# Kernel optimization log

Hardware: AMD Instinct MI355X
Metric: run time of the kernel (lower is better)

Reference implementation:

```python
import jax, jax.numpy as jnp
import numpy as np

B, N, D = 16, 1024, 512
H, KD = 8, 64
SCALE = 1.0 / np.sqrt(KD)


def setup_inputs() -> dict:
    key = jax.random.key(0)
    ks = jax.random.split(key, 6)
    return {
        "x": jax.random.normal(ks[0], (B, N, D), dtype=jnp.float32),
        "leadlag_bias": jax.random.normal(ks[1], (N, N), dtype=jnp.float32),
        "Wq": jax.random.normal(ks[2], (D, H * KD), dtype=jnp.float32) * 0.02,
        "Wk": jax.random.normal(ks[3], (D, H * KD), dtype=jnp.float32) * 0.02,
        "Wv": jax.random.normal(ks[4], (D, H * KD), dtype=jnp.float32) * 0.02,
        "Wo": jax.random.normal(ks[5], (H * KD, D), dtype=jnp.float32) * 0.02,
        "bias_scale": jnp.ones((H,), dtype=jnp.float32),
    }


def reference(x, leadlag_bias, Wq, Wk, Wv, Wo, bias_scale):
    # x: [B, N, D]; project and split heads -> [B, H, N, KD]
    def split_heads(t):
        return t.reshape(B, N, H, KD).transpose(0, 2, 1, 3)

    Q = split_heads(x @ Wq)
    K = split_heads(x @ Wk)
    V = split_heads(x @ Wv)

    # scores: [B, H, N, N] with per-head scaled additive lead-lag bias
    scores = jnp.einsum("bhqd,bhkd->bhqk", Q, K) * SCALE
    scores = scores + leadlag_bias[None, None, :, :] * bias_scale.reshape(1, H, 1, 1)

    attn = jax.nn.softmax(scores, axis=-1)  # dropout rate 0.0 / inference
    out = jnp.einsum("bhqk,bhkd->bhqd", attn, V)
    out = out.transpose(0, 2, 1, 3).reshape(B, N, H * KD)
    return out @ Wo
```

## Files before the change

### kernel.cpp

```cpp
#include <hip/hip_runtime.h>


#define DEV static __device__ __forceinline__

typedef __attribute__((ext_vector_type(8))) __bf16 bf16x8;
typedef __attribute__((ext_vector_type(4))) float f32x4;
typedef __attribute__((ext_vector_type(8))) unsigned short u16x8;

static constexpr float SCALE = 0.125f;
static constexpr float LOG2E = 1.4426950408889634f;
static constexpr float SM_SHIFT = 24.0f;
static constexpr int LDT = 72;

DEV unsigned short f2bf(float f) {
    unsigned int u = __builtin_bit_cast(unsigned int, f);
    u += 0x7FFFu + ((u >> 16) & 1u);
    return (unsigned short)(u >> 16);
}
DEV float bf2f(unsigned short u) {
    return __builtin_bit_cast(float, (unsigned int)u << 16);
}

DEV f32x4 mfma16(bf16x8 a, bf16x8 b, f32x4 c) {
    return __builtin_amdgcn_mfma_f32_16x16x32_bf16(a, b, c, 0, 0, 0);
}

__global__ __launch_bounds__(256) void prep_wt(
    const float* __restrict__ Wq, const float* __restrict__ Wk,
    const float* __restrict__ Wv, const float* __restrict__ Wo,
    const float* __restrict__ bias,
    unsigned short* __restrict__ Wt, unsigned short* __restrict__ Wot,
    unsigned short* __restrict__ BiasB)
{
    const int bid = blockIdx.x;
    const int tid = threadIdx.x;

    if (bid >= 256) {
        const int base = (bid - 256) * 2048 + tid * 8;
        float4 a = *(const float4*)(bias + base);
        float4 b = *(const float4*)(bias + base + 4);
        ushort4 u0 = make_ushort4(f2bf(a.x), f2bf(a.y), f2bf(a.z), f2bf(a.w));
        ushort4 u1 = make_ushort4(f2bf(b.x), f2bf(b.y), f2bf(b.z), f2bf(b.w));
        *(ushort4*)&BiasB[base] = u0;
        *(ushort4*)&BiasB[base + 4] = u1;
        return;
    }

    const int mat  = bid >> 6;
    const int tile = bid & 63;
    const int k0 = (tile >> 3) << 6;
    const int n0 = (tile & 7) << 6;
    const float* src = mat == 0 ? Wq : mat == 1 ? Wk : mat == 2 ? Wv : Wo;
    const float mul = (mat == 0) ? SCALE * LOG2E : 1.0f;

    __shared__ unsigned short T[64 * 68];

    #pragma unroll
    for (int i = 0; i < 4; ++i) {
        int idx = tid + (i << 8);
        int r = idx >> 4, c4 = (idx & 15) << 2;
        float4 v = *(const float4*)(src + (size_t)(k0 + r) * 512 + n0 + c4);
        T[r * 68 + c4 + 0] = f2bf(v.x * mul);
        T[r * 68 + c4 + 1] = f2bf(v.y * mul);
        T[r * 68 + c4 + 2] = f2bf(v.z * mul);
        T[r * 68 + c4 + 3] = f2bf(v.w * mul);
    }
    __syncthreads();
    unsigned short* dst = (mat < 3) ? (Wt + (size_t)(mat * 512) * 512) : Wot;
    #pragma unroll
    for (int i = 0; i < 4; ++i) {
        int idx = tid + (i << 8);
        int nr = idx >> 4, kc4 = (idx & 15) << 2;
        ushort4 u;
        u.x = T[(kc4 + 0) * 68 + nr];
        u.y = T[(kc4 + 1) * 68 + nr];
        u.z = T[(kc4 + 2) * 68 + nr];
        u.w = T[(kc4 + 3) * 68 + nr];
        *(ushort4*)&dst[(size_t)(n0 + nr) * 512 + k0 + kc4] = u;
    }
}

__global__ __launch_bounds__(256) void proj_gemm(
    const float* __restrict__ X,
    const unsigned short* __restrict__ Wt,
    unsigned short* __restrict__ Qb,
    unsigned short* __restrict__ Kb,
    unsigned short* __restrict__ Vtb)
{
    __shared__ unsigned short smem[2 * 128 * LDT];
    unsigned short* As = smem;
    unsigned short* Bs = smem + 128 * LDT;

    const int tid  = threadIdx.x;
    const int lane = tid & 63;
    const int wave = tid >> 6;
    const int wm = wave >> 1, wn = wave & 1;
    const int bm = blockIdx.x & 127, bn = blockIdx.x >> 7;
    const int m0 = bm << 7, n0 = bn << 7;
    const int gcol = lane & 15;
    const int grow = (lane >> 4) << 2;
    const int g8   = (lane >> 4) << 3;

    f32x4 acc[4][4];
    const f32x4 zf = {0.f, 0.f, 0.f, 0.f};
    #pragma unroll
    for (int i = 0; i < 4; ++i)
        #pragma unroll
        for (int j = 0; j < 4; ++j) acc[i][j] = zf;

    for (int kt = 0; kt < 8; ++kt) {
        const int k0 = kt << 6;
        #pragma unroll
        for (int i = 0; i < 8; ++i) {
            int idx = tid + (i << 8);
            int r = idx >> 4, c4 = (idx & 15) << 2;
            float4 v = *(const float4*)(X + (size_t)(m0 + r) * 512 + k0 + c4);
            ushort4 u = make_ushort4(f2bf(v.x), f2bf(v.y), f2bf(v.z), f2bf(v.w));
            *(ushort4*)&As[r * LDT + c4] = u;
            *(ushort4*)&Bs[r * LDT + c4] =
                *(const ushort4*)(Wt + (size_t)(n0 + r) * 512 + k0 + c4);
        }
        __syncthreads();
        #pragma unroll
        for (int ks = 0; ks < 2; ++ks) {
            bf16x8 af[4], bfr[4];
            #pragma unroll
            for (int f = 0; f < 4; ++f) {
                af[f]  = *(const bf16x8*)&As[(wm * 64 + f * 16 + gcol) * LDT + ks * 32 + g8];
                bfr[f] = *(const bf16x8*)&Bs[(wn * 64 + f * 16 + gcol) * LDT + ks * 32 + g8];
            }
            #pragma unroll
            for (int mf = 0; mf < 4; ++mf)
                #pragma unroll
                for (int nf = 0; nf < 4; ++nf)
                    acc[mf][nf] = mfma16(af[mf], bfr[nf], acc[mf][nf]);
        }
        __syncthreads();
    }

    const int sect = n0 >> 9;
    const int nq   = n0 & 511;
    const int b    = m0 >> 10;
    const int qb   = m0 & 1023;

    if (sect < 2) {
        unsigned short* dst = (sect == 0) ? Qb : Kb;
        #pragma unroll
        for (int mf = 0; mf < 4; ++mf)
            #pragma unroll
            for (int nf = 0; nf < 4; ++nf) {
                int ncol = nq + wn * 64 + nf * 16;
                int h = ncol >> 6;
                int d = (ncol & 63) + gcol;
                int q = qb + wm * 64 + mf * 16 + grow;
                unsigned short* p = dst + ((size_t)((b * 8 + h) * 1024 + q)) * 64 + d;
                #pragma unroll
                for (int r = 0; r < 4; ++r) p[r * 64] = f2bf(acc[mf][nf][r]);
            }
    } else {
        unsigned short* Ct = smem;
        const int CTP = 130;
        #pragma unroll
        for (int mf = 0; mf < 4; ++mf)
            #pragma unroll
            for (int nf = 0; nf < 4; ++nf) {
                int rr = wm * 64 + mf * 16 + grow;
                int cc = wn * 64 + nf * 16 + gcol;
                #pragma unroll
                for (int r = 0; r < 4; ++r)
                    Ct[(rr + r) * CTP + cc] = f2bf(acc[mf][nf][r]);
            }
        __syncthreads();
        const int qloc = tid & 127, half = tid >> 7;
        for (int it = 0; it < 64; ++it) {
            int dl = it * 2 + half;
            int ncol = nq + dl;
            int h = ncol >> 6, d = ncol & 63;
            Vtb[((size_t)((b * 8 + h) * 64 + d)) * 1024 + qb + qloc] = Ct[qloc * CTP + dl];
        }
    }
}

__global__ __launch_bounds__(256, 4) void attn_kernel(
    const unsigned short* __restrict__ Qb,
    const unsigned short* __restrict__ Kb,
    const unsigned short* __restrict__ Vtb,
    const unsigned short* __restrict__ BiasB,
    const float* __restrict__ bscale,
    unsigned short* __restrict__ AO)
{
    __shared__ unsigned short Klds[64 * LDT];
    __shared__ unsigned short Vlds[64 * LDT];
    __shared__ unsigned short Plds[128 * LDT];

    const int bid = blockIdx.x;
    const int G  = bid & 127;
    const int qt = bid >> 7;
    const int h  = G & 7, b = G >> 3;
    const int q0 = qt << 7;
    const int tid  = threadIdx.x;
    const int lane = tid & 63;
    const int wave = tid >> 6;
    const int wq   = wave << 5;
    const int gcol = lane & 15;
    const int grow = (lane >> 4) << 2;
    const int g8   = (lane >> 4) << 3;

    const float bs = bscale[h] * LOG2E;
    const unsigned short* Qp = Qb + ((size_t)((b * 8 + h) * 1024 + q0)) * 64;
    const unsigned short* Kp = Kb + (size_t)(b * 8 + h) * 1024 * 64;
    const unsigned short* Vp = Vtb + (size_t)(b * 8 + h) * 64 * 1024;
    const unsigned short* Bp = BiasB + (size_t)(q0 + wq) * 1024;

    #pragma unroll
    for (int i = 0; i < 4; ++i) {
        int idx = tid + (i << 8);
        int r = idx >> 3, c8 = (idx & 7) << 3;
        *(u16x8*)&Plds[r * LDT + c8] = *(const u16x8*)&Qp[(size_t)r * 64 + c8];
    }
    __syncthreads();
    bf16x8 qf[2][2];
    #pragma unroll
    for (int mf = 0; mf < 2; ++mf)
        #pragma unroll
        for (int ks = 0; ks < 2; ++ks)
            qf[mf][ks] = *(const bf16x8*)&Plds[(wq + mf * 16 + gcol) * LDT + ks * 32 + g8];
    __syncthreads();

    const f32x4 zf = {0.f, 0.f, 0.f, 0.f};
    f32x4 O[2][4];
    float psum[2][4];
    #pragma unroll
    for (int mf = 0; mf < 2; ++mf) {
        #pragma unroll
        for (int df = 0; df < 4; ++df) O[mf][df] = zf;
        #pragma unroll
        for (int r = 0; r < 4; ++r) psum[mf][r] = 0.f;
    }

    for (int t = 0; t < 16; ++t) {
        const int k0 = t << 6;
        #pragma unroll
        for (int i = 0; i < 2; ++i) {
            int idx = tid + (i << 8);
            int r = idx >> 3, c8 = (idx & 7) << 3;
            *(u16x8*)&Klds[r * LDT + c8] = *(const u16x8*)&Kp[(size_t)(k0 + r) * 64 + c8];
            *(u16x8*)&Vlds[r * LDT + c8] = *(const u16x8*)&Vp[(size_t)r * 1024 + k0 + c8];
        }
        #pragma unroll
        for (int pass = 0; pass < 4; ++pass) {
            int rl = (lane >> 3) + (pass << 3);
            int c8 = (lane & 7) << 3;
            *(u16x8*)&Plds[(wq + rl) * LDT + c8] =
                *(const u16x8*)&Bp[(size_t)rl * 1024 + k0 + c8];
        }
        __syncthreads();

        f32x4 s[2][4];
        #pragma unroll
        for (int mf = 0; mf < 2; ++mf)
            #pragma unroll
            for (int f = 0; f < 4; ++f) s[mf][f] = zf;
        #pragma unroll
        for (int ks = 0; ks < 2; ++ks) {
            bf16x8 kf_[4];
            #pragma unroll
            for (int f = 0; f < 4; ++f)
                kf_[f] = *(const bf16x8*)&Klds[(f * 16 + gcol) * LDT + ks * 32 + g8];
            #pragma unroll
            for (int mf = 0; mf < 2; ++mf)
                #pragma unroll
                for (int f = 0; f < 4; ++f)
                    s[mf][f] = mfma16(qf[mf][ks], kf_[f], s[mf][f]);
        }

        #pragma unroll
        for (int mf = 0; mf < 2; ++mf)
            #pragma unroll
            for (int f = 0; f < 4; ++f) {
                #pragma unroll
                for (int r = 0; r < 4; ++r) {
                    int a = (wq + mf * 16 + grow + r) * LDT + f * 16 + gcol;
                    float bv = bf2f(Plds[a]);
                    float e = exp2f(s[mf][f][r] + bv * bs - SM_SHIFT);
                    psum[mf][r] += e;
                    Plds[a] = f2bf(e);
                }
            }

        #pragma unroll
        for (int ks = 0; ks < 2; ++ks) {
            bf16x8 pa[2], vb[4];
            #pragma unroll
            for (int mf = 0; mf < 2; ++mf)
                pa[mf] = *(const bf16x8*)&Plds[(wq + mf * 16 + gcol) * LDT + ks * 32 + g8];
            #pragma unroll
            for (int df = 0; df < 4; ++df)
                vb[df] = *(const bf16x8*)&Vlds[(df * 16 + gcol) * LDT + ks * 32 + g8];
            #pragma unroll
            for (int mf = 0; mf < 2; ++mf)
                #pragma unroll
                for (int df = 0; df < 4; ++df)
                    O[mf][df] = mfma16(pa[mf], vb[df], O[mf][df]);
        }
        __syncthreads();
    }

    #pragma unroll
    for (int mf = 0; mf < 2; ++mf)
        #pragma unroll
        for (int r = 0; r < 4; ++r) {
            float rs = psum[mf][r];
            #pragma unroll
            for (int off = 1; off < 16; off <<= 1) rs += __shfl_xor(rs, off);
            float inv = 1.0f / rs;
            int q = q0 + wq + mf * 16 + grow + r;
            size_t base = ((size_t)(b * 1024 + q) << 9) + h * 64;
            #pragma unroll
            for (int df = 0; df < 4; ++df)
                AO[base + df * 16 + gcol] = f2bf(O[mf][df][r] * inv);
        }
}

__global__ __launch_bounds__(256) void out_gemm(
    const unsigned short* __restrict__ AOp,
    const unsigned short* __restrict__ Wot,
    float* __restrict__ Out)
{
    __shared__ unsigned short smem[2 * 128 * LDT];
    unsigned short* As = smem;
    unsigned short* Bs = smem + 128 * LDT;

    const int tid  = threadIdx.x;
    const int lane = tid & 63;
    const int wave = tid >> 6;
    const int wm = wave >> 1, wn = wave & 1;
    const int bm = blockIdx.x & 127, bn = blockIdx.x >> 7;
    const int m0 = bm << 7, n0 = bn << 7;
    const int gcol = lane & 15;
    const int grow = (lane >> 4) << 2;
    const int g8   = (lane >> 4) << 3;

    f32x4 acc[4][4];
    const f32x4 zf = {0.f, 0.f, 0.f, 0.f};
    #pragma unroll
    for (int i = 0; i < 4; ++i)
        #pragma unroll
        for (int j = 0; j < 4; ++j) acc[i][j] = zf;

    for (int kt = 0; kt < 8; ++kt) {
        const int k0 = kt << 6;
        #pragma unroll
        for (int i = 0; i < 8; ++i) {
            int idx = tid + (i << 8);
            int r = idx >> 4, c4 = (idx & 15) << 2;
            *(ushort4*)&As[r * LDT + c4] =
                *(const ushort4*)(AOp + (size_t)(m0 + r) * 512 + k0 + c4);
            *(ushort4*)&Bs[r * LDT + c4] =
                *(const ushort4*)(Wot + (size_t)(n0 + r) * 512 + k0 + c4);
        }
        __syncthreads();
        #pragma unroll
        for (int ks = 0; ks < 2; ++ks) {
            bf16x8 af[4], bfr[4];
            #pragma unroll
            for (int f = 0; f < 4; ++f) {
                af[f]  = *(const bf16x8*)&As[(wm * 64 + f * 16 + gcol) * LDT + ks * 32 + g8];
                bfr[f] = *(const bf16x8*)&Bs[(wn * 64 + f * 16 + gcol) * LDT + ks * 32 + g8];
            }
            #pragma unroll
            for (int mf = 0; mf < 4; ++mf)
                #pragma unroll
                for (int nf = 0; nf < 4; ++nf)
                    acc[mf][nf] = mfma16(af[mf], bfr[nf], acc[mf][nf]);
        }
        __syncthreads();
    }

    #pragma unroll
    for (int mf = 0; mf < 4; ++mf)
        #pragma unroll
        for (int nf = 0; nf < 4; ++nf) {
            int m = m0 + wm * 64 + mf * 16 + grow;
            int n = n0 + wn * 64 + nf * 16 + gcol;
            #pragma unroll
            for (int r = 0; r < 4; ++r)
                Out[(size_t)(m + r) * 512 + n] = acc[mf][nf][r];
        }
}

extern "C" void kernel_launch(void* const* d_in, const int* in_sizes, int n_in,
                              void* d_out, int out_size, void* d_ws, size_t ws_size,
                              hipStream_t stream)
{
    const float* x    = (const float*)d_in[0];
    const float* bias = (const float*)d_in[1];
    const float* Wq   = (const float*)d_in[2];
    const float* Wk   = (const float*)d_in[3];
    const float* Wv   = (const float*)d_in[4];
    const float* Wo   = (const float*)d_in[5];
    const float* bsc  = (const float*)d_in[6];
    float* out = (float*)d_out;

    char* ws = (char*)d_ws;
    const size_t MB = 1024 * 1024;
    unsigned short* Wt    = (unsigned short*)(ws);
    unsigned short* Wot   = (unsigned short*)(ws + 1536 * 512 * 2);
    unsigned short* BiasB = (unsigned short*)(ws + 2 * MB);
    unsigned short* Qb    = (unsigned short*)(ws + 4 * MB);
    unsigned short* Kb    = (unsigned short*)(ws + 20 * MB);
    unsigned short* Vtb   = (unsigned short*)(ws + 36 * MB);
    unsigned short* AOb   = (unsigned short*)(ws + 52 * MB);

    prep_wt  <<<768,  256, 0, stream>>>(Wq, Wk, Wv, Wo, bias, Wt, Wot, BiasB);
    proj_gemm<<<1536, 256, 0, stream>>>(x, Wt, Qb, Kb, Vtb);
    attn_kernel<<<1024, 256, 0, stream>>>(Qb, Kb, Vtb, BiasB, bsc, AOb);
    out_gemm <<<512,  256, 0, stream>>>(AOb, Wot, out);
}
```

Measured before the change: 285.5 us.

## Pre-convert X to bf16, transpose bias, and load bias/Q directly from global

The prep kernel now also converts x to bf16 once and writes a transposed bf16 bias, so each lane can read its four bias values as one ushort4 in MFMA layout. The attention kernel drops the bias and Q staging through LDS, along with two barriers, and reads both directly from global. The projection and output GEMMs switch to 16-byte vector loads of bf16 operands and no longer convert x inside the K loop. The cost is an extra global bf16 copy of x, which reuses the AO workspace region and relies on proj_gemm finishing before attention writes AO, plus uncoalesced bias reads in the attention inner loop.

New measurement: 253.7 us. -11.1%, faster.

```diff
diff --git a/kernel.cpp b/kernel.cpp
--- a/kernel.cpp
+++ b/kernel.cpp
@@ -28,21 +28,52 @@
 __global__ __launch_bounds__(256) void prep_wt(
     const float* __restrict__ Wq, const float* __restrict__ Wk,
     const float* __restrict__ Wv, const float* __restrict__ Wo,
-    const float* __restrict__ bias,
+    const float* __restrict__ bias, const float* __restrict__ X,
     unsigned short* __restrict__ Wt, unsigned short* __restrict__ Wot,
-    unsigned short* __restrict__ BiasB)
+    unsigned short* __restrict__ BiasT, unsigned short* __restrict__ Xb)
 {
     const int bid = blockIdx.x;
     const int tid = threadIdx.x;
 
+    if (bid >= 512) {
+        const size_t base = (size_t)(bid - 512) * 4096 + tid * 16;
+        #pragma unroll
+        for (int j = 0; j < 4; ++j) {
+            float4 v = *(const float4*)(X + base + j * 4);
+            *(ushort4*)&Xb[base + j * 4] =
+                make_ushort4(f2bf(v.x), f2bf(v.y), f2bf(v.z), f2bf(v.w));
+        }
+        return;
+    }
+
+    __shared__ unsigned short T[64 * 68];
+
     if (bid >= 256) {
-        const int base = (bid - 256) * 2048 + tid * 8;
-        float4 a = *(const float4*)(bias + base);
-        float4 b = *(const float4*)(bias + base + 4);
-        ushort4 u0 = make_ushort4(f2bf(a.x), f2bf(a.y), f2bf(a.z), f2bf(a.w));
-        ushort4 u1 = make_ushort4(f2bf(b.x), f2bf(b.y), f2bf(b.z), f2bf(b.w));
-        *(ushort4*)&BiasB[base] = u0;
-        *(ushort4*)&BiasB[base + 4] = u1;
+        const int tb = bid - 256;
+        const int q0 = (tb >> 4) << 6;
+        const int k0 = (tb & 15) << 6;
+        #pragma unroll
+        for (int i = 0; i < 4; ++i) {
+            int idx = tid + (i << 8);
+            int r = idx >> 4, c4 = (idx & 15) << 2;
+            float4 v = *(const float4*)(bias + (size_t)(q0 + r) * 1024 + k0 + c4);
+            T[r * 68 + c4 + 0] = f2bf(v.x);
+            T[r * 68 + c4 + 1] = f2bf(v.y);
+            T[r * 68 + c4 + 2] = f2bf(v.z);
+            T[r * 68 + c4 + 3] = f2bf(v.w);
+        }
+        __syncthreads();
+        #pragma unroll
+        for (int i = 0; i < 4; ++i) {
+            int idx = tid + (i << 8);
+            int kr = idx >> 4, qc4 = (idx & 15) << 2;
+            ushort4 u;
+            u.x = T[(qc4 + 0) * 68 + kr];
+            u.y = T[(qc4 + 1) * 68 + kr];
+            u.z = T[(qc4 + 2) * 68 + kr];
+            u.w = T[(qc4 + 3) * 68 + kr];
+            *(ushort4*)&BiasT[(size_t)(k0 + kr) * 1024 + q0 + qc4] = u;
+        }
         return;
     }
 
@@ -52,8 +83,6 @@
     const int n0 = (tile & 7) << 6;
     const float* src = mat == 0 ? Wq : mat == 1 ? Wk : mat == 2 ? Wv : Wo;
     const float mul = (mat == 0) ? SCALE * LOG2E : 1.0f;
-
-    __shared__ unsigned short T[64 * 68];
 
     #pragma unroll
     for (int i = 0; i < 4; ++i) {
@@ -81,7 +110,7 @@
 }
 
 __global__ __launch_bounds__(256) void proj_gemm(
-    const float* __restrict__ X,
+    const unsigned short* __restrict__ Xb,
     const unsigned short* __restrict__ Wt,
     unsigned short* __restrict__ Qb,
     unsigned short* __restrict__ Kb,
@@ -111,14 +140,13 @@
     for (int kt = 0; kt < 8; ++kt) {
         const int k0 = kt << 6;
         #pragma unroll
-        for (int i = 0; i < 8; ++i) {
+        for (int i = 0; i < 4; ++i) {
             int idx = tid + (i << 8);
-            int r = idx >> 4, c4 = (idx & 15) << 2;
-            float4 v = *(const float4*)(X + (size_t)(m0 + r) * 512 + k0 + c4);
-            ushort4 u = make_ushort4(f2bf(v.x), f2bf(v.y), f2bf(v.z), f2bf(v.w));
-            *(ushort4*)&As[r * LDT + c4] = u;
-            *(ushort4*)&Bs[r * LDT + c4] =
-                *(const ushort4*)(Wt + (size_t)(n0 + r) * 512 + k0 + c4);
+            int r = idx >> 3, c8 = (idx & 7) << 3;
+            *(u16x8*)&As[r * LDT + c8] =
+                *(const u16x8*)(Xb + (size_t)(m0 + r) * 512 + k0 + c8);
+            *(u16x8*)&Bs[r * LDT + c8] =
+                *(const u16x8*)(Wt + (size_t)(n0 + r) * 512 + k0 + c8);
         }
         __syncthreads();
         #pragma unroll
@@ -185,7 +213,7 @@
     const unsigned short* __restrict__ Qb,
     const unsigned short* __restrict__ Kb,
     const unsigned short* __restrict__ Vtb,
-    const unsigned short* __restrict__ BiasB,
+    const unsigned short* __restrict__ BiasT,
     const float* __restrict__ bscale,
     unsigned short* __restrict__ AO)
 {
@@ -210,22 +238,13 @@
     const unsigned short* Qp = Qb + ((size_t)((b * 8 + h) * 1024 + q0)) * 64;
     const unsigned short* Kp = Kb + (size_t)(b * 8 + h) * 1024 * 64;
     const unsigned short* Vp = Vtb + (size_t)(b * 8 + h) * 64 * 1024;
-    const unsigned short* Bp = BiasB + (size_t)(q0 + wq) * 1024;
-
-    #pragma unroll
-    for (int i = 0; i < 4; ++i) {
-        int idx = tid + (i << 8);
-        int r = idx >> 3, c8 = (idx & 7) << 3;
-        *(u16x8*)&Plds[r * LDT + c8] = *(const u16x8*)&Qp[(size_t)r * 64 + c8];
-    }
-    __syncthreads();
+
     bf16x8 qf[2][2];
     #pragma unroll
     for (int mf = 0; mf < 2; ++mf)
         #pragma unroll
         for (int ks = 0; ks < 2; ++ks)
-            qf[mf][ks] = *(const bf16x8*)&Plds[(wq + mf * 16 + gcol) * LDT + ks * 32 + g8];
-    __syncthreads();
+            qf[mf][ks] = *(const bf16x8*)&Qp[(size_t)(wq + mf * 16 + gcol) * 64 + ks * 32 + g8];
 
     const f32x4 zf = {0.f, 0.f, 0.f, 0.f};
     f32x4 O[2][4];
@@ -247,13 +266,6 @@
             *(u16x8*)&Klds[r * LDT + c8] = *(const u16x8*)&Kp[(size_t)(k0 + r) * 64 + c8];
             *(u16x8*)&Vlds[r * LDT + c8] = *(const u16x8*)&Vp[(size_t)r * 1024 + k0 + c8];
         }
-        #pragma unroll
-        for (int pass = 0; pass < 4; ++pass) {
-            int rl = (lane >> 3) + (pass << 3);
-            int c8 = (lane & 7) << 3;
-            *(u16x8*)&Plds[(wq + rl) * LDT + c8] =
-                *(const u16x8*)&Bp[(size_t)rl * 1024 + k0 + c8];
-        }
         __syncthreads();
 
         f32x4 s[2][4];
@@ -278,14 +290,21 @@
         for (int mf = 0; mf < 2; ++mf)
             #pragma unroll
             for (int f = 0; f < 4; ++f) {
-                #pragma unroll
-                for (int r = 0; r < 4; ++r) {
-                    int a = (wq + mf * 16 + grow + r) * LDT + f * 16 + gcol;
-                    float bv = bf2f(Plds[a]);
-                    float e = exp2f(s[mf][f][r] + bv * bs - SM_SHIFT);
-                    psum[mf][r] += e;
-                    Plds[a] = f2bf(e);
-                }
+                ushort4 b4 = *(const ushort4*)&BiasT[
+                    (size_t)(k0 + f * 16 + gcol) * 1024 + q0 + wq + mf * 16 + grow];
+                float bv0 = bf2f(b4.x), bv1 = bf2f(b4.y),
+                      bv2 = bf2f(b4.z), bv3 = bf2f(b4.w);
+                float e0 = exp2f(s[mf][f][0] + bv0 * bs - SM_SHIFT);
+                float e1 = exp2f(s[mf][f][1] + bv1 * bs - SM_SHIFT);
+                float e2 = exp2f(s[mf][f][2] + bv2 * bs - SM_SHIFT);
+                float e3 = exp2f(s[mf][f][3] + bv3 * bs - SM_SHIFT);
+                psum[mf][0] += e0; psum[mf][1] += e1;
+                psum[mf][2] += e2; psum[mf][3] += e3;
+                int a = (wq + mf * 16 + grow) * LDT + f * 16 + gcol;
+                Plds[a          ] = f2bf(e0);
+                Plds[a + LDT    ] = f2bf(e1);
+                Plds[a + 2 * LDT] = f2bf(e2);
+                Plds[a + 3 * LDT] = f2bf(e3);
             }
 
         #pragma unroll
@@ -351,13 +370,13 @@
     for (int kt = 0; kt < 8; ++kt) {
         const int k0 = kt << 6;
         #pragma unroll
-        for (int i = 0; i < 8; ++i) {
+        for (int i = 0; i < 4; ++i) {
             int idx = tid + (i << 8);
-            int r = idx >> 4, c4 = (idx & 15) << 2;
-            *(ushort4*)&As[r * LDT + c4] =
-                *(const ushort4*)(AOp + (size_t)(m0 + r) * 512 + k0 + c4);
-            *(ushort4*)&Bs[r * LDT + c4] =
-                *(const ushort4*)(Wot + (size_t)(n0 + r) * 512 + k0 + c4);
+            int r = idx >> 3, c8 = (idx & 7) << 3;
+            *(u16x8*)&As[r * LDT + c8] =
+                *(const u16x8*)(AOp + (size_t)(m0 + r) * 512 + k0 + c8);
+            *(u16x8*)&Bs[r * LDT + c8] =
+                *(const u16x8*)(Wot + (size_t)(n0 + r) * 512 + k0 + c8);
         }
         __syncthreads();
         #pragma unroll
@@ -406,14 +425,15 @@
     const size_t MB = 1024 * 1024;
     unsigned short* Wt    = (unsigned short*)(ws);
     unsigned short* Wot   = (unsigned short*)(ws + 1536 * 512 * 2);
-    unsigned short* BiasB = (unsigned short*)(ws + 2 * MB);
+    unsigned short* BiasT = (unsigned short*)(ws + 2 * MB);
     unsigned short* Qb    = (unsigned short*)(ws + 4 * MB);
     unsigned short* Kb    = (unsigned short*)(ws + 20 * MB);
     unsigned short* Vtb   = (unsigned short*)(ws + 36 * MB);
+    unsigned short* Xb    = (unsigned short*)(ws + 52 * MB);
     unsigned short* AOb   = (unsigned short*)(ws + 52 * MB);
 
-    prep_wt  <<<768,  256, 0, stream>>>(Wq, Wk, Wv, Wo, bias, Wt, Wot, BiasB);
-    proj_gemm<<<1536, 256, 0, stream>>>(x, Wt, Qb, Kb, Vtb);
-    attn_kernel<<<1024, 256, 0, stream>>>(Qb, Kb, Vtb, BiasB, bsc, AOb);
+    prep_wt  <<<2560, 256, 0, stream>>>(Wq, Wk, Wv, Wo, bias, x, Wt, Wot, BiasT, Xb);
+    proj_gemm<<<1536, 256, 0, stream>>>(Xb, Wt, Qb, Kb, Vtb);
+    attn_kernel<<<1024, 256, 0, stream>>>(Qb, Kb, Vtb, BiasT, bsc, AOb);
     out_gemm <<<512,  256, 0, stream>>>(AOb, Wot, out);
 }
```
